# Performance work log

Hardware: AMD Instinct MI355X
Metric: run time of the kernel (lower is better)

Reference implementation:

```python
import jax, jax.numpy as jnp
import numpy as np

B, T, F, U, NCLS = 128, 500, 64, 512, 11
R_ON = 0.05      # time-gate open ratio (Phased LSTM default)
ALPHA = 0.001    # leak rate when the gate is closed


def setup_inputs() -> dict:
    key = jax.random.key(0)
    ks = jax.random.split(key, 16)
    s4 = 1.0 / np.sqrt(F + U)
    inp = {
        "inputs": jax.random.normal(ks[0], (B, T, F), dtype=jnp.float32),
        "times": jax.random.uniform(ks[1], (B, T), dtype=jnp.float32) * 100.0,
        # PhasedLSTM cell 0 (input dim F)
        "k0": jax.random.normal(ks[2], (F, 4 * U), dtype=jnp.float32) * s4,
        "rk0": jax.random.normal(ks[3], (U, 4 * U), dtype=jnp.float32) * s4,
        "b0": jnp.zeros((4 * U,), dtype=jnp.float32),
        "tau0": jax.random.uniform(ks[4], (U,), dtype=jnp.float32, minval=1.0, maxval=10.0),
        "s0": jax.random.uniform(ks[5], (U,), dtype=jnp.float32, minval=0.0, maxval=10.0),
        # PhasedLSTM cell 1 (input dim U)
        "k1": jax.random.normal(ks[6], (U, 4 * U), dtype=jnp.float32) * s4,
        "rk1": jax.random.normal(ks[7], (U, 4 * U), dtype=jnp.float32) * s4,
        "b1": jnp.zeros((4 * U,), dtype=jnp.float32),
        "tau1": jax.random.uniform(ks[8], (U,), dtype=jnp.float32, minval=1.0, maxval=10.0),
        "s1": jax.random.uniform(ks[9], (U,), dtype=jnp.float32, minval=0.0, maxval=10.0),
        # classifier head
        "wfc": jax.random.normal(ks[10], (U, NCLS), dtype=jnp.float32) * (1.0 / np.sqrt(U)),
        "bfc": jnp.zeros((NCLS,), dtype=jnp.float32),
    }
    return inp


def _time_gate(t, tau, shift):
    # t: [B]; tau, shift: [U] -> k: [B, U]
    phi = jnp.mod(t[:, None] - shift[None, :], tau[None, :]) / tau[None, :]
    k = jnp.where(
        phi < 0.5 * R_ON,
        2.0 * phi / R_ON,
        jnp.where(phi < R_ON, 2.0 - 2.0 * phi / R_ON, ALPHA * phi),
    )
    return k


def _plstm_step(x, t, h, c, kern, rkern, bias, tau, shift):
    z = x @ kern + h @ rkern + bias                 # [B, 4U]
    i, f, g, o = jnp.split(z, 4, axis=-1)
    i, f, o = jax.nn.sigmoid(i), jax.nn.sigmoid(f), jax.nn.sigmoid(o)
    g = jnp.tanh(g)
    c_tilde = f * c + i * g
    h_tilde = o * jnp.tanh(c_tilde)
    kt = _time_gate(t, tau, shift)                  # [B, U]
    c_new = kt * c_tilde + (1.0 - kt) * c
    h_new = kt * h_tilde + (1.0 - kt) * h
    return h_new, c_new


def reference(inputs, times, k0, rk0, b0, tau0, s0, k1, rk1, b1, tau1, s1, wfc, bfc):
    x_t = jnp.transpose(inputs, (1, 0, 2))  # [T, B, F]
    t_t = jnp.transpose(times, (1, 0))      # [T, B]
    b = inputs.shape[0]
    u = rk0.shape[0]
    init = (jnp.zeros((b, u), jnp.float32), jnp.zeros((b, u), jnp.float32),
            jnp.zeros((b, u), jnp.float32), jnp.zeros((b, u), jnp.float32))

    def step(carry, xt):
        h0, c0, h1, c1 = carry
        x, t = xt
        h0, c0 = _plstm_step(x, t, h0, c0, k0, rk0, b0, tau0, s0)
        h1, c1 = _plstm_step(h0, t, h1, c1, k1, rk1, b1, tau1, s1)
        # dropout is identity at inference (training=False default)
        logits = h1 @ wfc + bfc
        probs = jax.nn.softmax(logits, axis=-1)
        return (h0, c0, h1, c1), probs

    _, out = jax.lax.scan(step, init, (x_t, t_t))   # out: [T, B, 11]
    return jnp.transpose(out, (1, 0, 2))            # [B, T, 11]
```

## Files before the change

kernel.cpp:

```cpp
#include <hip/hip_runtime.h>
#include <math.h>

namespace {

typedef __attribute__((ext_vector_type(8))) short s8b;
typedef __attribute__((ext_vector_type(4))) float f4;
typedef unsigned long long u64;

constexpr int B_ = 128;
constexpr int T_ = 500;
constexpr int F_ = 64;
constexpr int U_ = 512;
constexpr int NCLS_ = 11;
constexpr int HU = B_ * U_;
constexpr float R_ON_ = 0.05f;
constexpr float ALPHA_ = 0.001f;

constexpr int GRID_BLOCKS = 192;
constexpr int NGRP = 24;
constexpr int GSZ = 8;
constexpr int NPH = 502;

__device__ __forceinline__ ushort bf16_rne(float f) {
  union { float f; unsigned u; } v; v.f = f;
  unsigned r = (v.u + 0x7fffu + ((v.u >> 16) & 1u)) >> 16;
  return (ushort)r;
}
__device__ __forceinline__ float bf16_f(ushort h) {
  union { unsigned u; float f; } v; v.u = ((unsigned)h) << 16; return v.f;
}

__device__ __forceinline__ void st_u64(ushort* p, u64 v) {
  __hip_atomic_store((u64*)p, v, __ATOMIC_RELAXED, __HIP_MEMORY_SCOPE_AGENT);
}
__device__ __forceinline__ u64 ld_u64(const ushort* p) {
  return __hip_atomic_load((const u64*)p, __ATOMIC_RELAXED, __HIP_MEMORY_SCOPE_AGENT);
}
__device__ __forceinline__ u64 pack4(const ushort* h) {
  return (u64)h[0] | ((u64)h[1] << 16) | ((u64)h[2] << 32) | ((u64)h[3] << 48);
}

#define LDFRAG(dst, src) \
  asm volatile("global_load_dwordx4 %0, %1, off sc0 sc1" : "=&v"(dst) : "v"(src))

__device__ __forceinline__ int foff(int b, int k) {
  return (((k >> 5) * 8 + (b >> 4)) * 64 + ((b & 15) | (((k >> 3) & 3) << 4))) * 8 + (k & 7);
}

__device__ __forceinline__ void phase_barrier(unsigned* grp, unsigned* root,
                                              unsigned* gen, int gid, unsigned ph) {
  asm volatile("s_waitcnt vmcnt(0)" ::: "memory");
  __syncthreads();
  if (threadIdx.x == 0) {
    const unsigned old =
        __hip_atomic_fetch_add(&grp[gid * 32], 1u, __ATOMIC_RELAXED, __HIP_MEMORY_SCOPE_AGENT);
    if (old == ph * GSZ + (GSZ - 1)) {
      const unsigned r =
          __hip_atomic_fetch_add(root, 1u, __ATOMIC_RELAXED, __HIP_MEMORY_SCOPE_AGENT);
      if (r == ph * NGRP + (NGRP - 1)) {
        __hip_atomic_store(gen, ph + 1u, __ATOMIC_RELAXED, __HIP_MEMORY_SCOPE_AGENT);
      }
    }
    unsigned it = 0;
    for (;;) {
      const unsigned cur = ((++it & 255u) == 0u)
          ? __hip_atomic_load(gen, __ATOMIC_ACQUIRE, __HIP_MEMORY_SCOPE_AGENT)
          : __hip_atomic_load(gen, __ATOMIC_RELAXED, __HIP_MEMORY_SCOPE_AGENT);
      if (cur >= ph + 1u) break;
      __builtin_amdgcn_s_sleep(2);
    }
  }
  __syncthreads();
}

template <int NKS>
__device__ __forceinline__ void load_weights(
    s8b (&wh)[NKS], s8b (&wl)[NKS],
    const float* __restrict__ W1, int K1, const float* __restrict__ W2,
    int n, int kbase, int krow)
{
#pragma unroll
  for (int ks = 0; ks < NKS; ++ks) {
#pragma unroll
    for (int j = 0; j < 8; ++j) {
      const int kg = kbase + ks * 32 + krow + j;
      const float* src = (kg < K1) ? (W1 + (size_t)kg * 2048)
                                   : (W2 + (size_t)(kg - K1) * 2048);
      const float wv = src[n];
      const ushort hi = bf16_rne(wv);
      const ushort lo = bf16_rne(wv - bf16_f(hi));
      wh[ks][j] = (short)hi;
      wl[ks][j] = (short)lo;
    }
  }
}

template <int NKS>
__device__ __forceinline__ void gemm_cell(
    const s8b (&wh)[NKS], const s8b (&wl)[NKS],
    const ushort* __restrict__ Ahi, const ushort* __restrict__ Alo,
    int kbbase, bool withx, int t, const float* __restrict__ inputs,
    int lane, float* __restrict__ z_s, int zrow)
{
  const int rbase = (lane >> 4) * 4;
  const int krow = (lane >> 4) * 8;
#pragma unroll
  for (int rt = 0; rt < 8; ++rt) {
    s8b sh[NKS], sl[NKS];
#pragma unroll
    for (int ks = 0; ks < NKS; ++ks) {
      if (withx && ks < 2) continue;
      const int e = (((kbbase + ks) * 8 + rt) * 64 + lane) * 8;
      LDFRAG(sh[ks], Ahi + e);
      LDFRAG(sl[ks], Alo + e);
    }
    if (withx) {
      const int row = rt * 16 + (lane & 15);
#pragma unroll
      for (int ks = 0; ks < 2; ++ks) {
        const float* xp = inputs + ((size_t)row * T_ + t) * F_ + ks * 32 + krow;
        const float4 v0 = *(const float4*)xp;
        const float4 v1 = *(const float4*)(xp + 4);
        const float xv[8] = {v0.x, v0.y, v0.z, v0.w, v1.x, v1.y, v1.z, v1.w};
#pragma unroll
        for (int j = 0; j < 8; ++j) {
          const ushort hi = bf16_rne(xv[j]);
          sh[ks][j] = (short)hi;
          sl[ks][j] = (short)bf16_rne(xv[j] - bf16_f(hi));
        }
      }
    }
    asm volatile("s_waitcnt vmcnt(0)" ::: "memory");
    __builtin_amdgcn_sched_barrier(0);
    f4 a0 = {0.f, 0.f, 0.f, 0.f};
    f4 a1 = {0.f, 0.f, 0.f, 0.f};
    f4 a2 = {0.f, 0.f, 0.f, 0.f};
#pragma unroll
    for (int ks = 0; ks < NKS; ++ks) {
      a0 = __builtin_amdgcn_mfma_f32_16x16x32_bf16(sh[ks], wh[ks], a0, 0, 0, 0);
      a1 = __builtin_amdgcn_mfma_f32_16x16x32_bf16(sl[ks], wh[ks], a1, 0, 0, 0);
      a2 = __builtin_amdgcn_mfma_f32_16x16x32_bf16(sh[ks], wl[ks], a2, 0, 0, 0);
    }
    const f4 red = a0 + a1 + a2;
#pragma unroll
    for (int j = 0; j < 4; ++j)
      atomicAdd(&z_s[zrow * 133 + rt * 16 + rbase + j], red[j]);
  }
}

template <int NU>
__device__ __forceinline__ void elem_update(
    const float* __restrict__ z_s, int b, int t, int u0,
    const float* __restrict__ bias, const float* __restrict__ tau,
    const float* __restrict__ shift, const float* __restrict__ timesT,
    float (&c8)[NU], float (&h8)[NU],
    ushort* __restrict__ hhi_w, ushort* __restrict__ hlo_w)
{
  const float tt = timesT[t * B_ + b];
  ushort vh[NU], vl[NU];
#pragma unroll
  for (int uu = 0; uu < NU; ++uu) {
    const int u = u0 + uu;
    const float zi = z_s[(4 * uu + 0) * 133 + b] + bias[u];
    const float zf = z_s[(4 * uu + 1) * 133 + b] + bias[512 + u];
    const float zg = z_s[(4 * uu + 2) * 133 + b] + bias[1024 + u];
    const float zo = z_s[(4 * uu + 3) * 133 + b] + bias[1536 + u];

    const float ig = 1.f / (1.f + expf(-zi));
    const float fg = 1.f / (1.f + expf(-zf));
    const float gg = tanhf(zg);
    const float og = 1.f / (1.f + expf(-zo));

    const float c_old = c8[uu];
    const float c_t = fg * c_old + ig * gg;
    const float h_t = og * tanhf(c_t);

    const float tau_u = tau[u];
    float phi = fmodf(tt - shift[u], tau_u);
    if (phi < 0.f) phi += tau_u;
    phi /= tau_u;
    float kt;
    if (phi < 0.5f * R_ON_)      kt = phi * (2.0f / R_ON_);
    else if (phi < R_ON_)        kt = 2.0f - phi * (2.0f / R_ON_);
    else                         kt = ALPHA_ * phi;

    const float cn = kt * c_t + (1.0f - kt) * c_old;
    const float hn = kt * h_t + (1.0f - kt) * h8[uu];
    c8[uu] = cn;
    h8[uu] = hn;
    const ushort hi = bf16_rne(hn);
    vh[uu] = hi;
    vl[uu] = bf16_rne(hn - bf16_f(hi));
  }
  const int base = foff(b, u0);
#pragma unroll
  for (int q = 0; q < NU / 4; ++q) {
    st_u64(hhi_w + base + 4 * q, pack4(&vh[4 * q]));
    st_u64(hlo_w + base + 4 * q, pack4(&vl[4 * q]));
  }
}

__global__ void init_kernel(unsigned* state_u32, const float* times, float* timesT,
                            unsigned* bar) {
  const int i = blockIdx.x * blockDim.x + threadIdx.x;
  if (i < 4 * HU) state_u32[i] = 0u;
  if (i < T_ * B_) {
    const int t = i >> 7, b = i & 127;
    timesT[i] = times[b * T_ + t];
  }
  if (i < 4096) bar[i] = 0u;
}

__global__ __launch_bounds__(256, 1) void plstm_kernel(
    const float* __restrict__ inputs,
    const float* __restrict__ k0, const float* __restrict__ rk0,
    const float* __restrict__ b0, const float* __restrict__ tau0, const float* __restrict__ s0,
    const float* __restrict__ k1, const float* __restrict__ rk1,
    const float* __restrict__ b1, const float* __restrict__ tau1, const float* __restrict__ s1,
    const float* __restrict__ wfc, const float* __restrict__ bfc,
    float* __restrict__ out,
    ushort* __restrict__ h0hi, ushort* __restrict__ h0lo,
    ushort* __restrict__ h1hi, ushort* __restrict__ h1lo,
    const float* __restrict__ timesT,
    unsigned* __restrict__ bar)
{
  __shared__ __align__(16) float z_s[32 * 133];
  __shared__ float cls_s[4][12];

  const int bid = blockIdx.x;
  const int tid = threadIdx.x;
  const int w = tid >> 6;
  const int lane = tid & 63;
  const int krow = (lane >> 4) * 8;
  const int gid = bid >> 3;
  unsigned* grp = bar;
  unsigned* root = bar + NGRP * 32;
  unsigned* gen = bar + NGRP * 32 + 32;

  if (bid < 64) {
    const int u0 = bid * 8;
    const int ct = w & 1;
    const int ksl = w >> 1;
    const int c_loc = ct * 16 + (lane & 15);
    const int n = (c_loc & 3) * 512 + u0 + (c_loc >> 2);
    s8b wh[9], wl[9];
    load_weights<9>(wh, wl, k0, 64, rk0, n, ksl * 288, krow);
    float c8[8], h8[8];
#pragma unroll
    for (int i = 0; i < 8; ++i) { c8[i] = 0.f; h8[i] = 0.f; }

    for (unsigned ph = 0; ph < NPH; ++ph) {
      const bool work = ph < T_;
      const bool clsw = ph >= 2;
      if (work) {
        for (int i = tid; i < 32 * 133; i += 256) z_s[i] = 0.f;
      }
      if (clsw) {
        const int r = w >> 1;
        const int bcls = 2 * bid + r;
        const int idx = ((w & 1) << 6) | lane;
        const int u = idx * 4;
        const size_t pcl = (size_t)((ph + 1) & 1) * HU;
        const int e = foff(bcls, u);
        const u64 hu = ld_u64(h1hi + pcl + e);
        const u64 lu = ld_u64(h1lo + pcl + e);
        float acc[NCLS_];
#pragma unroll
        for (int c = 0; c < NCLS_; ++c) acc[c] = 0.f;
#pragma unroll
        for (int j = 0; j < 4; ++j) {
          const float h = bf16_f((ushort)(hu >> (16 * j))) + bf16_f((ushort)(lu >> (16 * j)));
          const float* wr = wfc + (size_t)(u + j) * NCLS_;
#pragma unroll
          for (int c = 0; c < NCLS_; ++c) acc[c] = fmaf(h, wr[c], acc[c]);
        }
#pragma unroll
        for (int off = 32; off >= 1; off >>= 1) {
#pragma unroll
          for (int c = 0; c < NCLS_; ++c) acc[c] += __shfl_xor(acc[c], off, 64);
        }
        if (lane == 0) {
#pragma unroll
          for (int c = 0; c < NCLS_; ++c) cls_s[w][c] = acc[c];
        }
      }
      __syncthreads();
      if (work) {
        const size_t rp = (size_t)(ph & 1) * HU;
        gemm_cell<9>(wh, wl, h0hi + rp, h0lo + rp, ksl ? 7 : -2,
                     ksl == 0, (int)ph, inputs, lane, z_s, c_loc);
      }
      __syncthreads();
      if (work && tid < 128) {
        const size_t wp = (size_t)((ph + 1) & 1) * HU;
        elem_update<8>(z_s, tid, (int)ph, u0, b0, tau0, s0, timesT,
                       c8, h8, h0hi + wp, h0lo + wp);
      }
      if (clsw && tid < 2) {
        const int t_cl = (int)ph - 2;
        const int bcls = 2 * bid + tid;
        float lg[NCLS_];
        float m = -1e30f;
#pragma unroll
        for (int c = 0; c < NCLS_; ++c) {
          lg[c] = cls_s[2 * tid][c] + cls_s[2 * tid + 1][c] + bfc[c];
          m = fmaxf(m, lg[c]);
        }
        float s = 0.f;
#pragma unroll
        for (int c = 0; c < NCLS_; ++c) { lg[c] = expf(lg[c] - m); s += lg[c]; }
        const float inv = 1.0f / s;
        float* op = out + ((size_t)bcls * T_ + t_cl) * NCLS_;
#pragma unroll
        for (int c = 0; c < NCLS_; ++c) op[c] = lg[c] * inv;
      }
      if (ph < NPH - 1) phase_barrier(grp, root, gen, gid, ph);
    }
  } else {
    const int cb = bid - 64;
    const int u0 = cb * 4;
    const int c_loc = lane & 15;
    const int n = (c_loc & 3) * 512 + u0 + (c_loc >> 2);
    s8b wh[8], wl[8];
    load_weights<8>(wh, wl, k1, 512, rk1, n, w * 256, krow);
    float c8[4], h8[4];
#pragma unroll
    for (int i = 0; i < 4; ++i) { c8[i] = 0.f; h8[i] = 0.f; }

    for (unsigned ph = 0; ph < NPH; ++ph) {
      const int t = (int)ph - 1;
      const bool work = (t >= 0 && t < T_);
      if (work) {
        for (int i = tid; i < 16 * 133; i += 256) z_s[i] = 0.f;
      }
      __syncthreads();
      if (work) {
        const ushort* Ahi;
        const ushort* Alo;
        int kbb;
        if (w < 2) {
          const size_t p = (size_t)(ph & 1) * HU;
          Ahi = h0hi + p; Alo = h0lo + p; kbb = w * 8;
        } else {
          const size_t p = (size_t)((ph + 1) & 1) * HU;
          Ahi = h1hi + p; Alo = h1lo + p; kbb = (w - 2) * 8;
        }
        gemm_cell<8>(wh, wl, Ahi, Alo, kbb, false, 0, inputs, lane, z_s, c_loc);
      }
      __syncthreads();
      if (work && tid < 128) {
        const size_t wp = (size_t)(ph & 1) * HU;
        elem_update<4>(z_s, tid, t, u0, b1, tau1, s1, timesT,
                       c8, h8, h1hi + wp, h1lo + wp);
      }
      if (ph < NPH - 1) phase_barrier(grp, root, gen, gid, ph);
    }
  }
}

}

extern "C" void kernel_launch(void* const* d_in, const int* in_sizes, int n_in,
                              void* d_out, int out_size, void* d_ws, size_t ws_size,
                              hipStream_t stream) {
  const float* inputs = (const float*)d_in[0];
  const float* times  = (const float*)d_in[1];
  const float* k0     = (const float*)d_in[2];
  const float* rk0    = (const float*)d_in[3];
  const float* b0     = (const float*)d_in[4];
  const float* tau0   = (const float*)d_in[5];
  const float* s0     = (const float*)d_in[6];
  const float* k1     = (const float*)d_in[7];
  const float* rk1    = (const float*)d_in[8];
  const float* b1     = (const float*)d_in[9];
  const float* tau1   = (const float*)d_in[10];
  const float* s1     = (const float*)d_in[11];
  const float* wfc    = (const float*)d_in[12];
  const float* bfc    = (const float*)d_in[13];
  float* out = (float*)d_out;

  ushort* h0hi = (ushort*)d_ws;
  ushort* h0lo = h0hi + 2 * HU;
  ushort* h1hi = h0lo + 2 * HU;
  ushort* h1lo = h1hi + 2 * HU;
  float* timesT = (float*)(h1lo + 2 * HU);
  unsigned* bar = (unsigned*)(timesT + T_ * B_);

  hipLaunchKernelGGL(init_kernel, dim3(1024), dim3(256), 0, stream,
                     (unsigned*)d_ws, times, timesT, bar);
  hipLaunchKernelGGL(plstm_kernel, dim3(GRID_BLOCKS), dim3(256), 0, stream,
                     inputs, k0, rk0, b0, tau0, s0,
                     k1, rk1, b1, tau1, s1, wfc, bfc, out,
                     h0hi, h0lo, h1hi, h1lo, timesT, bar);
}
```

Before: 10.38 ms.

## Double block width to 512 threads and software-pipeline cell-1 fragment loads

Each persistent block now runs 8 waves instead of 4, and the batch row tiles are split between two halves of the waves, so each wave handles 4 row tiles instead of 8. This shortens the serial per-step GEMM chain. The layer-1 path also double-buffers its fragment loads, issuing the loads for the next row tile before running the MFMAs on the current one with partial vmcnt waits, to hide global-load latency. The cost is twice as many register-resident weight copies per block, more LDS atomic contention, and higher register pressure under launch_bounds(512,2).

Result: no change. 10.45 ms (+0.7%).

```diff
diff --git a/kernel.cpp b/kernel.cpp
--- a/kernel.cpp
+++ b/kernel.cpp
@@ -42,6 +42,11 @@
 
 #define LDFRAG(dst, src) \
   asm volatile("global_load_dwordx4 %0, %1, off sc0 sc1" : "=&v"(dst) : "v"(src))
+
+#define WAITN(N) do { \
+  asm volatile("s_waitcnt vmcnt(" #N ")" ::: "memory"); \
+  __builtin_amdgcn_sched_barrier(0); \
+} while (0)
 
 __device__ __forceinline__ int foff(int b, int k) {
   return (((k >> 5) * 8 + (b >> 4)) * 64 + ((b & 15) | (((k >> 3) & 3) << 4))) * 8 + (k & 7);
@@ -96,16 +101,17 @@
 }
 
 template <int NKS>
-__device__ __forceinline__ void gemm_cell(
+__device__ __forceinline__ void gemm_c0(
     const s8b (&wh)[NKS], const s8b (&wl)[NKS],
     const ushort* __restrict__ Ahi, const ushort* __restrict__ Alo,
     int kbbase, bool withx, int t, const float* __restrict__ inputs,
-    int lane, float* __restrict__ z_s, int zrow)
+    int lane, float* __restrict__ z_s, int zrow, int rtbase)
 {
   const int rbase = (lane >> 4) * 4;
   const int krow = (lane >> 4) * 8;
 #pragma unroll
-  for (int rt = 0; rt < 8; ++rt) {
+  for (int r = 0; r < 4; ++r) {
+    const int rt = rtbase + r;
     s8b sh[NKS], sl[NKS];
 #pragma unroll
     for (int ks = 0; ks < NKS; ++ks) {
@@ -130,8 +136,7 @@
         }
       }
     }
-    asm volatile("s_waitcnt vmcnt(0)" ::: "memory");
-    __builtin_amdgcn_sched_barrier(0);
+    WAITN(0);
     f4 a0 = {0.f, 0.f, 0.f, 0.f};
     f4 a1 = {0.f, 0.f, 0.f, 0.f};
     f4 a2 = {0.f, 0.f, 0.f, 0.f};
@@ -146,6 +151,22 @@
     for (int j = 0; j < 4; ++j)
       atomicAdd(&z_s[zrow * 133 + rt * 16 + rbase + j], red[j]);
   }
+}
+
+__device__ __forceinline__ void mm8(
+    const s8b (&sh)[8], const s8b (&sl)[8],
+    const s8b (&wh)[8], const s8b (&wl)[8], f4& out)
+{
+  f4 a0 = {0.f, 0.f, 0.f, 0.f};
+  f4 a1 = {0.f, 0.f, 0.f, 0.f};
+  f4 a2 = {0.f, 0.f, 0.f, 0.f};
+#pragma unroll
+  for (int ks = 0; ks < 8; ++ks) {
+    a0 = __builtin_amdgcn_mfma_f32_16x16x32_bf16(sh[ks], wh[ks], a0, 0, 0, 0);
+    a1 = __builtin_amdgcn_mfma_f32_16x16x32_bf16(sl[ks], wh[ks], a1, 0, 0, 0);
+    a2 = __builtin_amdgcn_mfma_f32_16x16x32_bf16(sh[ks], wl[ks], a2, 0, 0, 0);
+  }
+  out = a0 + a1 + a2;
 }
 
 template <int NU>
@@ -211,7 +232,7 @@
   if (i < 4096) bar[i] = 0u;
 }
 
-__global__ __launch_bounds__(256, 1) void plstm_kernel(
+__global__ __launch_bounds__(512, 2) void plstm_kernel(
     const float* __restrict__ inputs,
     const float* __restrict__ k0, const float* __restrict__ rk0,
     const float* __restrict__ b0, const float* __restrict__ tau0, const float* __restrict__ s0,
@@ -240,7 +261,8 @@
   if (bid < 64) {
     const int u0 = bid * 8;
     const int ct = w & 1;
-    const int ksl = w >> 1;
+    const int ksl = (w >> 1) & 1;
+    const int rh = w >> 2;
     const int c_loc = ct * 16 + (lane & 15);
     const int n = (c_loc & 3) * 512 + u0 + (c_loc >> 2);
     s8b wh[9], wl[9];
@@ -253,9 +275,9 @@
       const bool work = ph < T_;
       const bool clsw = ph >= 2;
       if (work) {
-        for (int i = tid; i < 32 * 133; i += 256) z_s[i] = 0.f;
-      }
-      if (clsw) {
+        for (int i = tid; i < 32 * 133; i += 512) z_s[i] = 0.f;
+      }
+      if (clsw && w < 4) {
         const int r = w >> 1;
         const int bcls = 2 * bid + r;
         const int idx = ((w & 1) << 6) | lane;
@@ -287,8 +309,8 @@
       __syncthreads();
       if (work) {
         const size_t rp = (size_t)(ph & 1) * HU;
-        gemm_cell<9>(wh, wl, h0hi + rp, h0lo + rp, ksl ? 7 : -2,
-                     ksl == 0, (int)ph, inputs, lane, z_s, c_loc);
+        gemm_c0<9>(wh, wl, h0hi + rp, h0lo + rp, ksl ? 7 : -2,
+                   ksl == 0, (int)ph, inputs, lane, z_s, c_loc, rh * 4);
       }
       __syncthreads();
       if (work && tid < 128) {
@@ -319,39 +341,74 @@
   } else {
     const int cb = bid - 64;
     const int u0 = cb * 4;
+    const int ksl = w & 3;
+    const int rh = w >> 2;
     const int c_loc = lane & 15;
+    const int rbase = (lane >> 4) * 4;
     const int n = (c_loc & 3) * 512 + u0 + (c_loc >> 2);
     s8b wh[8], wl[8];
-    load_weights<8>(wh, wl, k1, 512, rk1, n, w * 256, krow);
-    float c8[4], h8[4];
-#pragma unroll
-    for (int i = 0; i < 4; ++i) { c8[i] = 0.f; h8[i] = 0.f; }
+    load_weights<8>(wh, wl, k1, 512, rk1, n, ksl * 256, krow);
+    float c4[4], h4[4];
+#pragma unroll
+    for (int i = 0; i < 4; ++i) { c4[i] = 0.f; h4[i] = 0.f; }
 
     for (unsigned ph = 0; ph < NPH; ++ph) {
       const int t = (int)ph - 1;
       const bool work = (t >= 0 && t < T_);
       if (work) {
-        for (int i = tid; i < 16 * 133; i += 256) z_s[i] = 0.f;
+        for (int i = tid; i < 16 * 133; i += 512) z_s[i] = 0.f;
       }
       __syncthreads();
       if (work) {
         const ushort* Ahi;
         const ushort* Alo;
         int kbb;
-        if (w < 2) {
+        if (ksl < 2) {
           const size_t p = (size_t)(ph & 1) * HU;
-          Ahi = h0hi + p; Alo = h0lo + p; kbb = w * 8;
+          Ahi = h0hi + p; Alo = h0lo + p; kbb = ksl * 8;
         } else {
           const size_t p = (size_t)((ph + 1) & 1) * HU;
-          Ahi = h1hi + p; Alo = h1lo + p; kbb = (w - 2) * 8;
-        }
-        gemm_cell<8>(wh, wl, Ahi, Alo, kbb, false, 0, inputs, lane, z_s, c_loc);
+          Ahi = h1hi + p; Alo = h1lo + p; kbb = (ksl - 2) * 8;
+        }
+        const int r0 = rh * 4;
+
+        s8b shA[8], slA[8], shB[8], slB[8];
+        f4 red;
+
+#define ISSUE8(SH, SL, RT) do { \
+  _Pragma("unroll") \
+  for (int ks_ = 0; ks_ < 8; ++ks_) { \
+    const int e_ = (((kbb + ks_) * 8 + (RT)) * 64 + lane) * 8; \
+    LDFRAG(SH[ks_], Ahi + e_); \
+    LDFRAG(SL[ks_], Alo + e_); \
+  } \
+} while (0)
+#define ZADD(V, RT) do { \
+  _Pragma("unroll") \
+  for (int j_ = 0; j_ < 4; ++j_) \
+    atomicAdd(&z_s[c_loc * 133 + (RT) * 16 + rbase + j_], (V)[j_]); \
+} while (0)
+
+        ISSUE8(shA, slA, r0);
+        ISSUE8(shB, slB, r0 + 1);
+        WAITN(16);
+        mm8(shA, slA, wh, wl, red); ZADD(red, r0);
+        ISSUE8(shA, slA, r0 + 2);
+        WAITN(16);
+        mm8(shB, slB, wh, wl, red); ZADD(red, r0 + 1);
+        ISSUE8(shB, slB, r0 + 3);
+        WAITN(16);
+        mm8(shA, slA, wh, wl, red); ZADD(red, r0 + 2);
+        WAITN(0);
+        mm8(shB, slB, wh, wl, red); ZADD(red, r0 + 3);
+#undef ISSUE8
+#undef ZADD
       }
       __syncthreads();
       if (work && tid < 128) {
         const size_t wp = (size_t)(ph & 1) * HU;
         elem_update<4>(z_s, tid, t, u0, b1, tau1, s1, timesT,
-                       c8, h8, h1hi + wp, h1lo + wp);
+                       c4, h4, h1hi + wp, h1lo + wp);
       }
       if (ph < NPH - 1) phase_barrier(grp, root, gen, gid, ph);
     }
@@ -388,7 +445,7 @@
 
   hipLaunchKernelGGL(init_kernel, dim3(1024), dim3(256), 0, stream,
                      (unsigned*)d_ws, times, timesT, bar);
-  hipLaunchKernelGGL(plstm_kernel, dim3(GRID_BLOCKS), dim3(256), 0, stream,
+  hipLaunchKernelGGL(plstm_kernel, dim3(GRID_BLOCKS), dim3(512), 0, stream,
                      inputs, k0, rk0, b0, tau0, s0,
                      k1, rk1, b1, tau1, s1, wfc, bfc, out,
                      h0hi, h0lo, h1hi, h1lo, timesT, bar);
```

## Switch recurrent GEMM to fp16 hi/lo split and shrink persistent grid

Applied to the files above, without the earlier changes.

Stores hidden states as a single fp16 array instead of bf16 hi/lo pairs and represents weights as fp16 hi plus a scaled fp16 lo. This cuts each step to two MFMAs instead of three and halves the hidden-state traffic. The persistent grid drops from 192 blocks of 256 threads to 64 blocks of 512 threads, and the barrier groups are reduced to match. The classifier is reworked into a per-wave row reduction. The risk is lower accuracy, since the activations are now one fp16 value with no residual term.

Result: slower. 15.85 ms (+52.8%).

```diff
diff --git a/kernel.cpp b/kernel.cpp
--- a/kernel.cpp
+++ b/kernel.cpp
@@ -3,7 +3,7 @@
 
 namespace {
 
-typedef __attribute__((ext_vector_type(8))) short s8b;
+typedef __attribute__((ext_vector_type(8))) _Float16 h8;
 typedef __attribute__((ext_vector_type(4))) float f4;
 typedef unsigned long long u64;
 
@@ -15,20 +15,16 @@
 constexpr int HU = B_ * U_;
 constexpr float R_ON_ = 0.05f;
 constexpr float ALPHA_ = 0.001f;
-
-constexpr int GRID_BLOCKS = 192;
-constexpr int NGRP = 24;
+constexpr float LO_SCALE = 1.0f / 2048.0f;
+
+constexpr int GRID_BLOCKS = 64;
+constexpr int NGRP = 8;
 constexpr int GSZ = 8;
 constexpr int NPH = 502;
 
-__device__ __forceinline__ ushort bf16_rne(float f) {
-  union { float f; unsigned u; } v; v.f = f;
-  unsigned r = (v.u + 0x7fffu + ((v.u >> 16) & 1u)) >> 16;
-  return (ushort)r;
-}
-__device__ __forceinline__ float bf16_f(ushort h) {
-  union { unsigned u; float f; } v; v.u = ((unsigned)h) << 16; return v.f;
-}
+union hu16 { ushort u; _Float16 h; };
+__device__ __forceinline__ ushort f2h_bits(float f) { hu16 v; v.h = (_Float16)f; return v.u; }
+__device__ __forceinline__ float h_bits2f(ushort b) { hu16 v; v.u = b; return (float)v.h; }
 
 __device__ __forceinline__ void st_u64(ushort* p, u64 v) {
   __hip_atomic_store((u64*)p, v, __ATOMIC_RELAXED, __HIP_MEMORY_SCOPE_AGENT);
@@ -40,8 +36,13 @@
   return (u64)h[0] | ((u64)h[1] << 16) | ((u64)h[2] << 32) | ((u64)h[3] << 48);
 }
 
-#define LDFRAG(dst, src) \
+#define LDH8(dst, src) \
   asm volatile("global_load_dwordx4 %0, %1, off sc0 sc1" : "=&v"(dst) : "v"(src))
+
+__device__ __forceinline__ void wait0() {
+  asm volatile("s_waitcnt vmcnt(0)" ::: "memory");
+  __builtin_amdgcn_sched_barrier(0);
+}
 
 __device__ __forceinline__ int foff(int b, int k) {
   return (((k >> 5) * 8 + (b >> 4)) * 64 + ((b & 15) | (((k >> 3) & 3) << 4))) * 8 + (k & 7);
@@ -74,8 +75,8 @@
 }
 
 template <int NKS>
-__device__ __forceinline__ void load_weights(
-    s8b (&wh)[NKS], s8b (&wl)[NKS],
+__device__ void load_weights_f16(
+    h8 (&wh)[NKS], h8 (&wl)[NKS],
     const float* __restrict__ W1, int K1, const float* __restrict__ W2,
     int n, int kbase, int krow)
 {
@@ -84,94 +85,38 @@
 #pragma unroll
     for (int j = 0; j < 8; ++j) {
       const int kg = kbase + ks * 32 + krow + j;
-      const float* src = (kg < K1) ? (W1 + (size_t)kg * 2048)
-                                   : (W2 + (size_t)(kg - K1) * 2048);
-      const float wv = src[n];
-      const ushort hi = bf16_rne(wv);
-      const ushort lo = bf16_rne(wv - bf16_f(hi));
-      wh[ks][j] = (short)hi;
-      wl[ks][j] = (short)lo;
-    }
-  }
-}
-
-template <int NKS>
-__device__ __forceinline__ void gemm_cell(
-    const s8b (&wh)[NKS], const s8b (&wl)[NKS],
-    const ushort* __restrict__ Ahi, const ushort* __restrict__ Alo,
-    int kbbase, bool withx, int t, const float* __restrict__ inputs,
-    int lane, float* __restrict__ z_s, int zrow)
-{
-  const int rbase = (lane >> 4) * 4;
-  const int krow = (lane >> 4) * 8;
-#pragma unroll
-  for (int rt = 0; rt < 8; ++rt) {
-    s8b sh[NKS], sl[NKS];
-#pragma unroll
-    for (int ks = 0; ks < NKS; ++ks) {
-      if (withx && ks < 2) continue;
-      const int e = (((kbbase + ks) * 8 + rt) * 64 + lane) * 8;
-      LDFRAG(sh[ks], Ahi + e);
-      LDFRAG(sl[ks], Alo + e);
-    }
-    if (withx) {
-      const int row = rt * 16 + (lane & 15);
-#pragma unroll
-      for (int ks = 0; ks < 2; ++ks) {
-        const float* xp = inputs + ((size_t)row * T_ + t) * F_ + ks * 32 + krow;
-        const float4 v0 = *(const float4*)xp;
-        const float4 v1 = *(const float4*)(xp + 4);
-        const float xv[8] = {v0.x, v0.y, v0.z, v0.w, v1.x, v1.y, v1.z, v1.w};
-#pragma unroll
-        for (int j = 0; j < 8; ++j) {
-          const ushort hi = bf16_rne(xv[j]);
-          sh[ks][j] = (short)hi;
-          sl[ks][j] = (short)bf16_rne(xv[j] - bf16_f(hi));
-        }
-      }
-    }
-    asm volatile("s_waitcnt vmcnt(0)" ::: "memory");
-    __builtin_amdgcn_sched_barrier(0);
-    f4 a0 = {0.f, 0.f, 0.f, 0.f};
-    f4 a1 = {0.f, 0.f, 0.f, 0.f};
-    f4 a2 = {0.f, 0.f, 0.f, 0.f};
-#pragma unroll
-    for (int ks = 0; ks < NKS; ++ks) {
-      a0 = __builtin_amdgcn_mfma_f32_16x16x32_bf16(sh[ks], wh[ks], a0, 0, 0, 0);
-      a1 = __builtin_amdgcn_mfma_f32_16x16x32_bf16(sl[ks], wh[ks], a1, 0, 0, 0);
-      a2 = __builtin_amdgcn_mfma_f32_16x16x32_bf16(sh[ks], wl[ks], a2, 0, 0, 0);
-    }
-    const f4 red = a0 + a1 + a2;
-#pragma unroll
-    for (int j = 0; j < 4; ++j)
-      atomicAdd(&z_s[zrow * 133 + rt * 16 + rbase + j], red[j]);
-  }
-}
-
-template <int NU>
-__device__ __forceinline__ void elem_update(
-    const float* __restrict__ z_s, int b, int t, int u0,
+      const float wv = (kg < K1) ? W1[(size_t)kg * 2048 + n]
+                                 : W2[(size_t)(kg - K1) * 2048 + n];
+      const _Float16 hi = (_Float16)wv;
+      wh[ks][j] = hi;
+      wl[ks][j] = (_Float16)((wv - (float)hi) * 2048.0f);
+    }
+  }
+}
+
+__device__ __forceinline__ void elem_update4(
+    const float* __restrict__ z_s, int b, int t, int u0, int uoff,
     const float* __restrict__ bias, const float* __restrict__ tau,
     const float* __restrict__ shift, const float* __restrict__ timesT,
-    float (&c8)[NU], float (&h8)[NU],
-    ushort* __restrict__ hhi_w, ushort* __restrict__ hlo_w)
+    float (&cc)[4], float (&hh)[4], ushort* __restrict__ hw)
 {
   const float tt = timesT[t * B_ + b];
-  ushort vh[NU], vl[NU];
-#pragma unroll
-  for (int uu = 0; uu < NU; ++uu) {
-    const int u = u0 + uu;
-    const float zi = z_s[(4 * uu + 0) * 133 + b] + bias[u];
-    const float zf = z_s[(4 * uu + 1) * 133 + b] + bias[512 + u];
-    const float zg = z_s[(4 * uu + 2) * 133 + b] + bias[1024 + u];
-    const float zo = z_s[(4 * uu + 3) * 133 + b] + bias[1536 + u];
+  ushort vh[4];
+#pragma unroll
+  for (int uu = 0; uu < 4; ++uu) {
+    const int ub = uoff + uu;
+    const int u = u0 + ub;
+    const float zi = z_s[(4 * ub + 0) * 133 + b] + bias[u];
+    const float zf = z_s[(4 * ub + 1) * 133 + b] + bias[512 + u];
+    const float zg = z_s[(4 * ub + 2) * 133 + b] + bias[1024 + u];
+    const float zo = z_s[(4 * ub + 3) * 133 + b] + bias[1536 + u];
 
     const float ig = 1.f / (1.f + expf(-zi));
     const float fg = 1.f / (1.f + expf(-zf));
     const float gg = tanhf(zg);
     const float og = 1.f / (1.f + expf(-zo));
 
-    const float c_old = c8[uu];
+    const float c_old = cc[uu];
     const float c_t = fg * c_old + ig * gg;
     const float h_t = og * tanhf(c_t);
 
@@ -185,25 +130,58 @@
     else                         kt = ALPHA_ * phi;
 
     const float cn = kt * c_t + (1.0f - kt) * c_old;
-    const float hn = kt * h_t + (1.0f - kt) * h8[uu];
-    c8[uu] = cn;
-    h8[uu] = hn;
-    const ushort hi = bf16_rne(hn);
-    vh[uu] = hi;
-    vl[uu] = bf16_rne(hn - bf16_f(hi));
-  }
-  const int base = foff(b, u0);
-#pragma unroll
-  for (int q = 0; q < NU / 4; ++q) {
-    st_u64(hhi_w + base + 4 * q, pack4(&vh[4 * q]));
-    st_u64(hlo_w + base + 4 * q, pack4(&vl[4 * q]));
+    const float hn = kt * h_t + (1.0f - kt) * hh[uu];
+    cc[uu] = cn;
+    hh[uu] = hn;
+    vh[uu] = f2h_bits(hn);
+  }
+  st_u64(hw + foff(b, u0 + uoff), pack4(vh));
+}
+
+__device__ __forceinline__ void classifier_row(
+    int b, int t, const ushort* __restrict__ h1p,
+    const float* __restrict__ wfc, const float* __restrict__ bfc,
+    float* __restrict__ out, int lane)
+{
+  const int u = lane * 8;
+  const int e = foff(b, u);
+  const u64 d0 = ld_u64(h1p + e);
+  const u64 d1 = ld_u64(h1p + e + 4);
+  float acc[NCLS_];
+#pragma unroll
+  for (int c = 0; c < NCLS_; ++c) acc[c] = 0.f;
+#pragma unroll
+  for (int j = 0; j < 8; ++j) {
+    const ushort hb = (ushort)(((j < 4) ? d0 : d1) >> (16 * (j & 3)));
+    const float h = h_bits2f(hb);
+    const float* wr = wfc + (size_t)(u + j) * NCLS_;
+#pragma unroll
+    for (int c = 0; c < NCLS_; ++c) acc[c] = fmaf(h, wr[c], acc[c]);
+  }
+#pragma unroll
+  for (int off = 32; off >= 1; off >>= 1) {
+#pragma unroll
+    for (int c = 0; c < NCLS_; ++c) acc[c] += __shfl_xor(acc[c], off, 64);
+  }
+  if (lane == 0) {
+    float lg[NCLS_];
+    float m = -1e30f;
+#pragma unroll
+    for (int c = 0; c < NCLS_; ++c) { lg[c] = acc[c] + bfc[c]; m = fmaxf(m, lg[c]); }
+    float s = 0.f;
+#pragma unroll
+    for (int c = 0; c < NCLS_; ++c) { lg[c] = expf(lg[c] - m); s += lg[c]; }
+    const float inv = 1.0f / s;
+    float* op = out + ((size_t)b * T_ + t) * NCLS_;
+#pragma unroll
+    for (int c = 0; c < NCLS_; ++c) op[c] = lg[c] * inv;
   }
 }
 
 __global__ void init_kernel(unsigned* state_u32, const float* times, float* timesT,
                             unsigned* bar) {
   const int i = blockIdx.x * blockDim.x + threadIdx.x;
-  if (i < 4 * HU) state_u32[i] = 0u;
+  if (i < 2 * HU) state_u32[i] = 0u;
   if (i < T_ * B_) {
     const int t = i >> 7, b = i & 127;
     timesT[i] = times[b * T_ + t];
@@ -211,7 +189,7 @@
   if (i < 4096) bar[i] = 0u;
 }
 
-__global__ __launch_bounds__(256, 1) void plstm_kernel(
+__global__ __launch_bounds__(512, 2) void plstm_kernel(
     const float* __restrict__ inputs,
     const float* __restrict__ k0, const float* __restrict__ rk0,
     const float* __restrict__ b0, const float* __restrict__ tau0, const float* __restrict__ s0,
@@ -219,139 +197,143 @@
     const float* __restrict__ b1, const float* __restrict__ tau1, const float* __restrict__ s1,
     const float* __restrict__ wfc, const float* __restrict__ bfc,
     float* __restrict__ out,
-    ushort* __restrict__ h0hi, ushort* __restrict__ h0lo,
-    ushort* __restrict__ h1hi, ushort* __restrict__ h1lo,
+    ushort* __restrict__ h0s, ushort* __restrict__ h1s,
     const float* __restrict__ timesT,
     unsigned* __restrict__ bar)
 {
-  __shared__ __align__(16) float z_s[32 * 133];
-  __shared__ float cls_s[4][12];
+  __shared__ __align__(16) float z_s[64 * 133];
 
   const int bid = blockIdx.x;
   const int tid = threadIdx.x;
   const int w = tid >> 6;
   const int lane = tid & 63;
+  const int ct = w & 3;
+  const int kh = w >> 2;
   const int krow = (lane >> 4) * 8;
+  const int c_loc = ct * 16 + (lane & 15);
+  const int rbase = (lane >> 4) * 4;
   const int gid = bid >> 3;
+  const int b_el = tid & 127;
+  const int uoff = (tid >> 7) * 4;
   unsigned* grp = bar;
   unsigned* root = bar + NGRP * 32;
-  unsigned* gen = bar + NGRP * 32 + 32;
-
-  if (bid < 64) {
-    const int u0 = bid * 8;
-    const int ct = w & 1;
-    const int ksl = w >> 1;
-    const int c_loc = ct * 16 + (lane & 15);
+  unsigned* gen = root + 32;
+
+  if (bid < 32) {
+    const int u0 = bid * 16;
     const int n = (c_loc & 3) * 512 + u0 + (c_loc >> 2);
-    s8b wh[9], wl[9];
-    load_weights<9>(wh, wl, k0, 64, rk0, n, ksl * 288, krow);
-    float c8[8], h8[8];
-#pragma unroll
-    for (int i = 0; i < 8; ++i) { c8[i] = 0.f; h8[i] = 0.f; }
+    h8 wh[9], wl[9];
+    load_weights_f16<9>(wh, wl, k0, 64, rk0, n, kh * 288, krow);
+    float cc[4], hh[4];
+#pragma unroll
+    for (int i = 0; i < 4; ++i) { cc[i] = 0.f; hh[i] = 0.f; }
 
     for (unsigned ph = 0; ph < NPH; ++ph) {
       const bool work = ph < T_;
-      const bool clsw = ph >= 2;
-      if (work) {
-        for (int i = tid; i < 32 * 133; i += 256) z_s[i] = 0.f;
-      }
-      if (clsw) {
-        const int r = w >> 1;
-        const int bcls = 2 * bid + r;
-        const int idx = ((w & 1) << 6) | lane;
-        const int u = idx * 4;
-        const size_t pcl = (size_t)((ph + 1) & 1) * HU;
-        const int e = foff(bcls, u);
-        const u64 hu = ld_u64(h1hi + pcl + e);
-        const u64 lu = ld_u64(h1lo + pcl + e);
-        float acc[NCLS_];
-#pragma unroll
-        for (int c = 0; c < NCLS_; ++c) acc[c] = 0.f;
-#pragma unroll
-        for (int j = 0; j < 4; ++j) {
-          const float h = bf16_f((ushort)(hu >> (16 * j))) + bf16_f((ushort)(lu >> (16 * j)));
-          const float* wr = wfc + (size_t)(u + j) * NCLS_;
-#pragma unroll
-          for (int c = 0; c < NCLS_; ++c) acc[c] = fmaf(h, wr[c], acc[c]);
+      if (work) {
+        for (int i = tid; i < 64 * 133; i += 512) z_s[i] = 0.f;
+      }
+      __syncthreads();
+      if (work) {
+        const ushort* A = h0s + (size_t)(ph & 1) * HU;
+#pragma unroll 1
+        for (int rt = 0; rt < 8; ++rt) {
+          h8 st[9];
+          f4 xr[4];
+#pragma unroll
+          for (int ks = 0; ks < 9; ++ks) {
+            if (kh == 0 && ks < 2) {
+              const float* xp = inputs +
+                  ((size_t)(rt * 16 + (lane & 15)) * T_ + ph) * F_ + ks * 32 + krow;
+              xr[2 * ks]     = *(const f4*)xp;
+              xr[2 * ks + 1] = *(const f4*)(xp + 4);
+            } else {
+              const int kb = (kh == 0) ? (ks - 2) : (7 + ks);
+              LDH8(st[ks], A + ((size_t)(kb * 8 + rt) * 64 + lane) * 8);
+            }
+          }
+          wait0();
+          if (kh == 0) {
+#pragma unroll
+            for (int ks = 0; ks < 2; ++ks) {
+#pragma unroll
+              for (int j = 0; j < 4; ++j) {
+                st[ks][j]     = (_Float16)xr[2 * ks][j];
+                st[ks][4 + j] = (_Float16)xr[2 * ks + 1][j];
+              }
+            }
+          }
+          f4 a0 = {0.f, 0.f, 0.f, 0.f};
+          f4 a1 = {0.f, 0.f, 0.f, 0.f};
+#pragma unroll
+          for (int ks = 0; ks < 9; ++ks) {
+            a0 = __builtin_amdgcn_mfma_f32_16x16x32_f16(st[ks], wh[ks], a0, 0, 0, 0);
+            a1 = __builtin_amdgcn_mfma_f32_16x16x32_f16(st[ks], wl[ks], a1, 0, 0, 0);
+          }
+          const f4 red = a0 + a1 * LO_SCALE;
+#pragma unroll
+          for (int j = 0; j < 4; ++j)
+            atomicAdd(&z_s[c_loc * 133 + rt * 16 + rbase + j], red[j]);
         }
-#pragma unroll
-        for (int off = 32; off >= 1; off >>= 1) {
-#pragma unroll
-          for (int c = 0; c < NCLS_; ++c) acc[c] += __shfl_xor(acc[c], off, 64);
-        }
-        if (lane == 0) {
-#pragma unroll
-          for (int c = 0; c < NCLS_; ++c) cls_s[w][c] = acc[c];
-        }
       }
       __syncthreads();
       if (work) {
-        const size_t rp = (size_t)(ph & 1) * HU;
-        gemm_cell<9>(wh, wl, h0hi + rp, h0lo + rp, ksl ? 7 : -2,
-                     ksl == 0, (int)ph, inputs, lane, z_s, c_loc);
-      }
-      __syncthreads();
-      if (work && tid < 128) {
-        const size_t wp = (size_t)((ph + 1) & 1) * HU;
-        elem_update<8>(z_s, tid, (int)ph, u0, b0, tau0, s0, timesT,
-                       c8, h8, h0hi + wp, h0lo + wp);
-      }
-      if (clsw && tid < 2) {
-        const int t_cl = (int)ph - 2;
-        const int bcls = 2 * bid + tid;
-        float lg[NCLS_];
-        float m = -1e30f;
-#pragma unroll
-        for (int c = 0; c < NCLS_; ++c) {
-          lg[c] = cls_s[2 * tid][c] + cls_s[2 * tid + 1][c] + bfc[c];
-          m = fmaxf(m, lg[c]);
-        }
-        float s = 0.f;
-#pragma unroll
-        for (int c = 0; c < NCLS_; ++c) { lg[c] = expf(lg[c] - m); s += lg[c]; }
-        const float inv = 1.0f / s;
-        float* op = out + ((size_t)bcls * T_ + t_cl) * NCLS_;
-#pragma unroll
-        for (int c = 0; c < NCLS_; ++c) op[c] = lg[c] * inv;
+        elem_update4(z_s, b_el, (int)ph, u0, uoff, b0, tau0, s0, timesT,
+                     cc, hh, h0s + (size_t)((ph + 1) & 1) * HU);
+      }
+      if (w < 4 && ph >= 2) {
+        classifier_row(bid * 4 + w, (int)ph - 2,
+                       h1s + (size_t)((ph + 1) & 1) * HU, wfc, bfc, out, lane);
       }
       if (ph < NPH - 1) phase_barrier(grp, root, gen, gid, ph);
     }
   } else {
-    const int cb = bid - 64;
-    const int u0 = cb * 4;
-    const int c_loc = lane & 15;
+    const int u0 = (bid - 32) * 16;
     const int n = (c_loc & 3) * 512 + u0 + (c_loc >> 2);
-    s8b wh[8], wl[8];
-    load_weights<8>(wh, wl, k1, 512, rk1, n, w * 256, krow);
-    float c8[4], h8[4];
-#pragma unroll
-    for (int i = 0; i < 4; ++i) { c8[i] = 0.f; h8[i] = 0.f; }
+    h8 wh[16], wl[16];
+    load_weights_f16<16>(wh, wl, k1, 512, rk1, n, kh * 512, krow);
+    float cc[4], hh[4];
+#pragma unroll
+    for (int i = 0; i < 4; ++i) { cc[i] = 0.f; hh[i] = 0.f; }
 
     for (unsigned ph = 0; ph < NPH; ++ph) {
       const int t = (int)ph - 1;
       const bool work = (t >= 0 && t < T_);
       if (work) {
-        for (int i = tid; i < 16 * 133; i += 256) z_s[i] = 0.f;
+        for (int i = tid; i < 64 * 133; i += 512) z_s[i] = 0.f;
       }
       __syncthreads();
       if (work) {
-        const ushort* Ahi;
-        const ushort* Alo;
-        int kbb;
-        if (w < 2) {
-          const size_t p = (size_t)(ph & 1) * HU;
-          Ahi = h0hi + p; Alo = h0lo + p; kbb = w * 8;
-        } else {
-          const size_t p = (size_t)((ph + 1) & 1) * HU;
-          Ahi = h1hi + p; Alo = h1lo + p; kbb = (w - 2) * 8;
+        const ushort* A = (kh == 0) ? h0s + (size_t)(ph & 1) * HU
+                                    : h1s + (size_t)((ph + 1) & 1) * HU;
+#pragma unroll 1
+        for (int rt = 0; rt < 8; ++rt) {
+          f4 a0 = {0.f, 0.f, 0.f, 0.f};
+          f4 a1 = {0.f, 0.f, 0.f, 0.f};
+#pragma unroll
+          for (int g = 0; g < 2; ++g) {
+            h8 st[8];
+#pragma unroll
+            for (int k8 = 0; k8 < 8; ++k8) {
+              LDH8(st[k8], A + ((size_t)((g * 8 + k8) * 8 + rt) * 64 + lane) * 8);
+            }
+            wait0();
+#pragma unroll
+            for (int k8 = 0; k8 < 8; ++k8) {
+              a0 = __builtin_amdgcn_mfma_f32_16x16x32_f16(st[k8], wh[g * 8 + k8], a0, 0, 0, 0);
+              a1 = __builtin_amdgcn_mfma_f32_16x16x32_f16(st[k8], wl[g * 8 + k8], a1, 0, 0, 0);
+            }
+          }
+          const f4 red = a0 + a1 * LO_SCALE;
+#pragma unroll
+          for (int j = 0; j < 4; ++j)
+            atomicAdd(&z_s[c_loc * 133 + rt * 16 + rbase + j], red[j]);
         }
-        gemm_cell<8>(wh, wl, Ahi, Alo, kbb, false, 0, inputs, lane, z_s, c_loc);
       }
       __syncthreads();
-      if (work && tid < 128) {
-        const size_t wp = (size_t)(ph & 1) * HU;
-        elem_update<4>(z_s, tid, t, u0, b1, tau1, s1, timesT,
-                       c8, h8, h1hi + wp, h1lo + wp);
+      if (work) {
+        elem_update4(z_s, b_el, t, u0, uoff, b1, tau1, s1, timesT,
+                     cc, hh, h1s + (size_t)(ph & 1) * HU);
       }
       if (ph < NPH - 1) phase_barrier(grp, root, gen, gid, ph);
     }
@@ -379,17 +361,15 @@
   const float* bfc    = (const float*)d_in[13];
   float* out = (float*)d_out;
 
-  ushort* h0hi = (ushort*)d_ws;
-  ushort* h0lo = h0hi + 2 * HU;
-  ushort* h1hi = h0lo + 2 * HU;
-  ushort* h1lo = h1hi + 2 * HU;
-  float* timesT = (float*)(h1lo + 2 * HU);
+  ushort* h0s = (ushort*)d_ws;
+  ushort* h1s = h0s + 2 * HU;
+  float* timesT = (float*)(h1s + 2 * HU);
   unsigned* bar = (unsigned*)(timesT + T_ * B_);
 
-  hipLaunchKernelGGL(init_kernel, dim3(1024), dim3(256), 0, stream,
+  hipLaunchKernelGGL(init_kernel, dim3(512), dim3(256), 0, stream,
                      (unsigned*)d_ws, times, timesT, bar);
-  hipLaunchKernelGGL(plstm_kernel, dim3(GRID_BLOCKS), dim3(256), 0, stream,
+  hipLaunchKernelGGL(plstm_kernel, dim3(GRID_BLOCKS), dim3(512), 0, stream,
                      inputs, k0, rk0, b0, tau0, s0,
                      k1, rk1, b1, tau1, s1, wfc, bfc, out,
-                     h0hi, h0lo, h1hi, h1lo, timesT, bar);
-}
+                     h0s, h1s, timesT, bar);
+}
```
